# Performance work log

Measured on AMD Instinct MI355X. Metric: run time of the kernel, lower is better.

Reference implementation:

```python
import jax, jax.numpy as jnp
import numpy as np

B = 4             # graphs per batch
POS_RANGE = 240.0 # pos lives in [0, 240)^3
VOXELS = (20.0, 30.0, 50.0, 80.0)
NEG = -1e30


def _basis(u):
    # open B-spline basis, degree 1, kernel_size 2, dim 3 -> 8 weights per edge
    cols = []
    for k in range(8):
        w = (u[:, 0] if k & 4 else 1.0 - u[:, 0])
        w = w * (u[:, 1] if k & 2 else 1.0 - u[:, 1])
        w = w * (u[:, 2] if k & 1 else 1.0 - u[:, 2])
        cols.append(w)
    return jnp.stack(cols, axis=1)  # [E, 8]


def _cartesian(pos, src, dst, emask):
    # T.Cartesian(cat=False, norm=True): rel pos scaled into [0,1]
    rel = pos[src] - pos[dst]
    m = jnp.max(jnp.where(emask[:, None], jnp.abs(rel), 0.0))
    return rel / (2.0 * jnp.maximum(m, 1e-9)) + 0.5


def _spline_conv(x, src, dst, pseudo, emask, W, Wr, b, n_nodes):
    # out_i = mean_{j->i} sum_k B_k(u_ij) x_j W_k + x_i Wr + b
    basis = _basis(pseudo) * emask[:, None].astype(x.dtype)  # [E,8]
    xk = jnp.einsum('ni,kio->nko', x, W)                     # [N,8,O]
    msg = basis[:, 0, None] * xk[src, 0]
    for k in range(1, 8):
        msg = msg + basis[:, k, None] * xk[src, k]           # [E,O]
    agg = jax.ops.segment_sum(msg, dst, num_segments=n_nodes)
    deg = jax.ops.segment_sum(emask.astype(x.dtype), dst, num_segments=n_nodes)
    return agg / jnp.maximum(deg, 1.0)[:, None] + x @ Wr + b


def _voxel_ids(pos, batch, vs):
    G = int(np.ceil(POS_RANGE / vs))
    c = jnp.clip(jnp.floor(pos / vs).astype(jnp.int64), 0, G - 1)
    cell = (c[:, 0] * G + c[:, 1]) * G + c[:, 2]
    return batch * (G ** 3) + cell, G ** 3


def _max_pool(x, pos, batch, valid, src, dst, emask, vs):
    # voxel-grid max pooling: nodes become fixed voxel cells (empty cells masked)
    nid, ncells = _voxel_ids(pos, batch, vs)
    n_new = B * ncells
    xm = jnp.where(valid[:, None], x, NEG)
    x_p = jax.ops.segment_max(xm, nid, num_segments=n_new)
    cnt = jax.ops.segment_sum(valid.astype(x.dtype), nid, num_segments=n_new)
    v_new = cnt > 0
    x_p = jnp.where(v_new[:, None], x_p, 0.0)
    pos_p = jax.ops.segment_sum(pos * valid[:, None].astype(pos.dtype), nid, num_segments=n_new)
    pos_p = pos_p / jnp.maximum(cnt, 1.0)[:, None]
    batch_p = jnp.arange(n_new, dtype=jnp.int64) // ncells
    # coarsen edges: remap to cells, drop self loops, coalesce at fixed size
    s2, d2 = nid[src], nid[dst]
    sent = n_new * n_new
    key = jnp.where(emask & (s2 != d2), s2 * n_new + d2, sent)
    uk = jnp.unique(key, size=key.shape[0], fill_value=sent)
    em = uk != sent
    uk = jnp.where(em, uk, 0)
    return x_p, pos_p, batch_p, v_new, uk // n_new, uk % n_new, em


def setup_inputs():
    key = jax.random.key(0)
    ks = jax.random.split(key, 24)
    NP, DEG = 5000, 8
    N = B * NP
    E = N * DEG
    x = jax.random.normal(ks[0], (N, 1), dtype=jnp.float32)
    pos = jax.random.uniform(ks[1], (N, 3), dtype=jnp.float32) * POS_RANGE
    src = jnp.repeat(jnp.arange(N, dtype=jnp.int64), DEG)
    delta = jax.random.randint(ks[2], (E,), 1, 100, dtype=jnp.int64)
    dst = (src // NP) * NP + (src % NP + delta) % NP   # intra-graph edges
    edge_index = jnp.stack([src, dst])
    batch = jnp.arange(N, dtype=jnp.int64) // NP
    sizes = [1, 64, 128, 256, 512]
    params = {}
    for l in range(4):
        ci, co = sizes[l], sizes[l + 1]
        params[f'W{l+1}'] = jax.random.normal(ks[3 + 3 * l], (8, ci, co), dtype=jnp.float32) / np.sqrt(8.0 * ci)
        params[f'Wr{l+1}'] = jax.random.normal(ks[4 + 3 * l], (ci, co), dtype=jnp.float32) / np.sqrt(float(ci))
        params[f'b{l+1}'] = jnp.zeros((co,), dtype=jnp.float32)
    params['fc1_w'] = jax.random.normal(ks[16], (64 * 512, 1024), dtype=jnp.float32) / np.sqrt(64.0 * 512.0)
    params['fc1_b'] = jnp.zeros((1024,), dtype=jnp.float32)
    params['fc2_w'] = jax.random.normal(ks[17], (1024, 1), dtype=jnp.float32) / np.sqrt(1024.0)
    params['fc2_b'] = jnp.zeros((1,), dtype=jnp.float32)
    return dict(x=x, pos=pos, edge_index=edge_index, batch=batch, **params)


def reference(x, pos, edge_index, batch, W1, Wr1, b1, W2, Wr2, b2, W3, Wr3, b3,
              W4, Wr4, b4, fc1_w, fc1_b, fc2_w, fc2_b):
    src, dst = edge_index[0], edge_index[1]
    n_nodes = x.shape[0]
    valid = jnp.ones((n_nodes,), dtype=bool)
    emask = jnp.ones((src.shape[0],), dtype=bool)
    Ws = [(W1, Wr1, b1), (W2, Wr2, b2), (W3, Wr3, b3), (W4, Wr4, b4)]
    for l in range(4):
        pseudo = _cartesian(pos, src, dst, emask)
        W, Wr, b = Ws[l]
        x = jax.nn.elu(_spline_conv(x, src, dst, pseudo, emask, W, Wr, b, n_nodes))
        if l < 3:
            x, pos, batch, valid, src, dst, emask = _max_pool(x, pos, batch, valid, src, dst, emask, VOXELS[l])
            n_nodes = x.shape[0]
    # MaxPoolingX(voxel=80, size=64): ceil(240/80)^3 = 27 <= 64 slots per graph
    nid, ncells = _voxel_ids(pos, batch, VOXELS[3])
    cluster = batch * 64 + (nid % ncells)
    xm = jnp.where(valid[:, None], x, NEG)
    xg = jax.ops.segment_max(xm, cluster, num_segments=B * 64)
    xg = jnp.where(xg <= NEG / 2, 0.0, xg)      # empty slots -> 0 (scatter-max default)
    xg = xg.reshape(B, 64 * 512)
    h = jax.nn.elu(xg @ fc1_w + fc1_b)           # dropout = identity (eval mode)
    return jax.nn.elu(h @ fc2_w + fc2_b)         # [B, 1]
```

## Files before the change

kernel.cpp:

```cpp
#include <hip/hip_runtime.h>

static constexpr int E0 = 160000;
static constexpr int NL0 = 20000;
static constexpr int NL1 = 6912;
static constexpr int NL2 = 2048;
static constexpr int NL3 = 500;

typedef short bf16x8 __attribute__((ext_vector_type(8)));
typedef float f32x4 __attribute__((ext_vector_type(4)));

__device__ __forceinline__ unsigned f2ord(float f) {
  unsigned u = __float_as_uint(f);
  return (u & 0x80000000u) ? ~u : (u | 0x80000000u);
}
__device__ __forceinline__ float ord2f(unsigned u) {
  unsigned v = (u & 0x80000000u) ? (u & 0x7fffffffu) : ~u;
  return __uint_as_float(v);
}
__device__ __forceinline__ float eluf(float x) { return x > 0.f ? x : expm1f(x); }
__device__ __forceinline__ void basis8(float u0, float u1, float u2, float* w) {
  float a0 = 1.f - u0, a1 = 1.f - u1, a2 = 1.f - u2;
  w[0] = a0*a1*a2; w[1] = a0*a1*u2; w[2] = a0*u1*a2; w[3] = a0*u1*u2;
  w[4] = u0*a1*a2; w[5] = u0*a1*u2; w[6] = u0*u1*a2; w[7] = u0*u1*u2;
}
__device__ __forceinline__ unsigned short f2b(float f) {
  unsigned u = __float_as_uint(f);
  return (unsigned short)((u + 0x7fffu + ((u >> 16) & 1u)) >> 16);
}
__device__ __forceinline__ float b2f(unsigned short h) {
  return __uint_as_float(((unsigned)h) << 16);
}
__device__ __forceinline__ int clampi(int v, int lo, int hi) {
  return v < lo ? lo : (v > hi ? hi : v);
}

__device__ __forceinline__ void mfma_tile(const unsigned short* __restrict__ Ah,
    const unsigned short* __restrict__ Al, const unsigned short* __restrict__ Bh,
    const unsigned short* __restrict__ Bl, int M, long K, int m0, int n0,
    int kbeg, int ksl, char* smem, f32x4* acc) {
  auto Ash = (unsigned short (*)[40])(smem);
  auto Asl = (unsigned short (*)[40])(smem + 5120);
  auto Bsh = (unsigned short (*)[40])(smem + 10240);
  auto Bsl = (unsigned short (*)[40])(smem + 15360);
  int t = threadIdx.x;
  int r = t >> 2, sg = (t & 3) * 8;
  int w = t >> 6, lane = t & 63;
  int ar = (w << 4) + (lane & 15), kq = (lane >> 4) << 3;
  for (int kt = 0; kt < ksl; kt += 32) {
    bf16x8 va = {}, vl = {};
    if (m0 + r < M) {
      long ga = (long)(m0 + r) * K + kbeg + kt + sg;
      va = *(const bf16x8*)&Ah[ga];
      vl = *(const bf16x8*)&Al[ga];
    }
    *(bf16x8*)&Ash[r][sg] = va;
    *(bf16x8*)&Asl[r][sg] = vl;
    long gb = (long)(n0 + r) * K + kbeg + kt + sg;
    *(bf16x8*)&Bsh[r][sg] = *(const bf16x8*)&Bh[gb];
    *(bf16x8*)&Bsl[r][sg] = *(const bf16x8*)&Bl[gb];
    __syncthreads();
    bf16x8 ah = *(const bf16x8*)&Ash[ar][kq];
    bf16x8 al = *(const bf16x8*)&Asl[ar][kq];
    #pragma unroll
    for (int nt = 0; nt < 4; nt++) {
      int br = (nt << 4) + (lane & 15);
      bf16x8 bh = *(const bf16x8*)&Bsh[br][kq];
      bf16x8 bl = *(const bf16x8*)&Bsl[br][kq];
      acc[nt] = __builtin_amdgcn_mfma_f32_16x16x32_bf16(al, bh, acc[nt], 0, 0, 0);
      acc[nt] = __builtin_amdgcn_mfma_f32_16x16x32_bf16(ah, bl, acc[nt], 0, 0, 0);
      acc[nt] = __builtin_amdgcn_mfma_f32_16x16x32_bf16(ah, bh, acc[nt], 0, 0, 0);
    }
    __syncthreads();
  }
}

__global__ __launch_bounds__(256)
void k_prep(const int* __restrict__ src0, const int* __restrict__ dst0,
            const float* __restrict__ pos0, const float* __restrict__ x0,
            int* __restrict__ degi, int4* __restrict__ erec0u, float* __restrict__ mbuf,
            const float* __restrict__ W1, const float* __restrict__ Wr1, float* __restrict__ wc1,
            const float* __restrict__ W2, const float* __restrict__ Wr2,
            const float* __restrict__ W3, const float* __restrict__ Wr3,
            const float* __restrict__ W4, const float* __restrict__ Wr4,
            unsigned short* __restrict__ w2h, unsigned short* __restrict__ w2l,
            unsigned short* __restrict__ w3h, unsigned short* __restrict__ w3l,
            unsigned short* __restrict__ w4h, unsigned short* __restrict__ w4l) {
  __shared__ __align__(16) float T[64][65];
  __shared__ float red[4];
  int tid = blockIdx.x * 256 + threadIdx.x, gsz = gridDim.x * 256;
  float v = 0.f;
  for (int e = tid; e < E0; e += gsz) {
    int s = src0[e], d = dst0[e];
    atomicAdd(&degi[d], 1);
    float r0 = pos0[s*3]   - pos0[d*3];
    float r1 = pos0[s*3+1] - pos0[d*3+1];
    float r2 = pos0[s*3+2] - pos0[d*3+2];
    erec0u[e] = make_int4(__float_as_int(x0[s]), __float_as_int(r0),
                          __float_as_int(r1), __float_as_int(r2));
    v = fmaxf(v, fmaxf(fabsf(r0), fmaxf(fabsf(r1), fabsf(r2))));
  }
  #pragma unroll
  for (int off = 32; off; off >>= 1) v = fmaxf(v, __shfl_down(v, off, 64));
  if ((threadIdx.x & 63) == 0) red[threadIdx.x >> 6] = v;
  __syncthreads();
  if (threadIdx.x == 0)
    atomicMax((unsigned*)mbuf,
              __float_as_uint(fmaxf(fmaxf(red[0], red[1]), fmaxf(red[2], red[3]))));
  for (int b = blockIdx.x; b < 378; b += gridDim.x) {
    const float *W, *Wr; unsigned short *oh, *ol; int K, N, kt, nt;
    if (b < 18)      { W = W2; Wr = Wr2; oh = w2h; ol = w2l; K = 576;  N = 128; kt = b / 2; nt = b % 2; }
    else if (b < 90) { int q = b - 18; W = W3; Wr = Wr3; oh = w3h; ol = w3l; K = 1152; N = 256; kt = q / 4; nt = q % 4; }
    else             { int q = b - 90; W = W4; Wr = Wr4; oh = w4h; ol = w4l; K = 2304; N = 512; kt = q / 8; nt = q % 8; }
    int k0 = kt * 64, n0 = nt * 64, KW = K - K / 9;
    __syncthreads();
    for (int i = threadIdx.x; i < 4096; i += 256) {
      int kk = i >> 6, nn = i & 63, k = k0 + kk;
      T[kk][nn] = (k < KW) ? W[(long)k * N + n0 + nn] : Wr[(long)(k - KW) * N + n0 + nn];
    }
    __syncthreads();
    for (int i = threadIdx.x; i < 4096; i += 256) {
      int nn = i >> 6, kk = i & 63;
      float vv = T[kk][nn];
      unsigned short hu = f2b(vv), lu = f2b(vv - b2f(hu));
      long o = (long)(n0 + nn) * K + k0 + kk;
      oh[o] = hu; ol[o] = lu;
    }
  }
  if (blockIdx.x == 0)
    for (int i = threadIdx.x; i < 576; i += 256)
      wc1[i] = (i < 512) ? W1[i] : Wr1[i - 512];
}

__global__ void k_alloc(int* __restrict__ degi, int* __restrict__ rowbeg,
                        int* __restrict__ rowlen, int* __restrict__ cursor,
                        int* __restrict__ ctr, int N) {
  int n = blockIdx.x * 256 + threadIdx.x;
  if (n >= N) return;
  int len = degi[n];
  int st = atomicAdd(ctr, len);
  rowbeg[n] = st; cursor[n] = st; rowlen[n] = len; degi[n] = 0;
}

__global__ void k_scat(const int4* __restrict__ eu, const int* __restrict__ du,
                       const int* __restrict__ ecnt, int ecap,
                       int* __restrict__ cursor, int4* __restrict__ es) {
  int n = ecnt ? *ecnt : ecap;
  for (int e = blockIdx.x * 256 + threadIdx.x; e < n; e += gridDim.x * 256) {
    int p = atomicAdd(&cursor[du[e]], 1);
    es[p] = eu[e];
  }
}

__global__ __launch_bounds__(256)
void k_l1a(const int4* __restrict__ erec, const int* __restrict__ rowbeg,
           const int* __restrict__ rowlen, const float* __restrict__ mbuf,
           float* __restrict__ ysg) {
  int t = threadIdx.x;
  int d = blockIdx.x * 32 + (t >> 3);
  if (d >= NL0) return;
  int sub = t & 7;
  float inv = 0.5f / fmaxf(mbuf[0], 1e-9f);
  int beg = rowbeg[d], len = rowlen[d], end = beg + len;
  float acc[8] = {};
  for (int j = beg + sub; j < end; j += 8) {
    int4 rc = erec[j];
    float xv = __int_as_float(rc.x);
    float w[8];
    basis8(__int_as_float(rc.y) * inv + 0.5f, __int_as_float(rc.z) * inv + 0.5f,
           __int_as_float(rc.w) * inv + 0.5f, w);
    #pragma unroll
    for (int k = 0; k < 8; k++) acc[k] += w[k] * xv;
  }
  #pragma unroll
  for (int m = 1; m < 8; m <<= 1)
    #pragma unroll
    for (int k = 0; k < 8; k++) acc[k] += __shfl_xor(acc[k], m, 64);
  if (sub == 0) {
    float sc = 1.f / fmaxf((float)len, 1.f);
    float4 o0 = make_float4(acc[0]*sc, acc[1]*sc, acc[2]*sc, acc[3]*sc);
    float4 o1 = make_float4(acc[4]*sc, acc[5]*sc, acc[6]*sc, acc[7]*sc);
    *(float4*)&ysg[d*8]     = o0;
    *(float4*)&ysg[d*8 + 4] = o1;
  }
}

__global__ __launch_bounds__(256)
void k_l1b(const float* __restrict__ ysg, const float* __restrict__ x0,
           const float* __restrict__ pos0, const float* __restrict__ wc1,
           const float* __restrict__ b1,
           unsigned* __restrict__ pord1, float* __restrict__ cnt1,
           float* __restrict__ possum1, int* __restrict__ nid) {
  int wv = threadIdx.x >> 6, lane = threadIdx.x & 63;
  int d = blockIdx.x * 4 + wv;
  if (d >= NL0) return;
  float wcol[9];
  #pragma unroll
  for (int k = 0; k < 8; k++) wcol[k] = wc1[k * 64 + lane];
  wcol[8] = wc1[512 + lane];
  float4 a0 = *(const float4*)&ysg[d*8];
  float4 a1 = *(const float4*)&ysg[d*8 + 4];
  float v = b1[lane] + x0[d] * wcol[8]
          + a0.x * wcol[0] + a0.y * wcol[1] + a0.z * wcol[2] + a0.w * wcol[3]
          + a1.x * wcol[4] + a1.y * wcol[5] + a1.z * wcol[6] + a1.w * wcol[7];
  v = eluf(v);
  float pd0 = pos0[d*3], pd1 = pos0[d*3+1], pd2 = pos0[d*3+2];
  int c0 = clampi((int)floorf(pd0 / 20.f), 0, 11);
  int c1 = clampi((int)floorf(pd1 / 20.f), 0, 11);
  int c2 = clampi((int)floorf(pd2 / 20.f), 0, 11);
  int id = (d / 5000) * 1728 + (c0 * 12 + c1) * 12 + c2;
  atomicMax(&pord1[(long)id * 64 + lane], f2ord(v));
  if (lane == 0) {
    nid[d] = id;
    atomicAdd(&cnt1[id], 1.f);
    atomicAdd(&possum1[id*3],   pd0);
    atomicAdd(&possum1[id*3+1], pd1);
    atomicAdd(&possum1[id*3+2], pd2);
  }
}

__global__ __launch_bounds__(256)
void k_pedge(const int4* __restrict__ erecf, const int* __restrict__ srcf,
             const int* __restrict__ dstf, const int* __restrict__ ecntf, int ecap,
             const int* __restrict__ nid, int Nn, unsigned* __restrict__ bitmap,
             int4* __restrict__ erecu, int* __restrict__ dstu, int* __restrict__ ecntc,
             int* __restrict__ degi, const float* __restrict__ possum,
             const float* __restrict__ cnt, float* __restrict__ mo) {
  __shared__ float red[4];
  int n = ecntf ? *ecntf : ecap;
  int lane = threadIdx.x & 63;
  int stride = gridDim.x * 256;
  float vmax = 0.f;
  for (int base = blockIdx.x * 256; base < n; base += stride) {
    int e = base + threadIdx.x;
    bool win = false;
    int s2 = 0, d2 = 0;
    float r0 = 0.f, r1 = 0.f, r2 = 0.f;
    if (e < n) {
      int sL = erecf ? erecf[e].x : srcf[e];
      int dL = dstf[e];
      s2 = nid[sL]; d2 = nid[dL];
      if (s2 != d2) {
        float ics = 1.f / fmaxf(cnt[s2], 1.f), icd = 1.f / fmaxf(cnt[d2], 1.f);
        r0 = possum[s2*3]   * ics - possum[d2*3]   * icd;
        r1 = possum[s2*3+1] * ics - possum[d2*3+1] * icd;
        r2 = possum[s2*3+2] * ics - possum[d2*3+2] * icd;
        vmax = fmaxf(vmax, fmaxf(fabsf(r0), fmaxf(fabsf(r1), fabsf(r2))));
        unsigned key = (unsigned)s2 * (unsigned)Nn + (unsigned)d2;
        unsigned bit = 1u << (key & 31);
        unsigned old = atomicOr(&bitmap[key >> 5], bit);
        win = !(old & bit);
      }
    }
    unsigned long long mask = __ballot(win);
    if (mask) {
      int leader = __ffsll((unsigned long long)mask) - 1;
      int bq = 0;
      if (lane == leader) bq = atomicAdd(ecntc, __popcll(mask));
      bq = __shfl(bq, leader, 64);
      if (win) {
        int q = bq + __popcll(mask & ((1ULL << lane) - 1ULL));
        erecu[q] = make_int4(s2, __float_as_int(r0), __float_as_int(r1), __float_as_int(r2));
        dstu[q] = d2;
        atomicAdd(&degi[d2], 1);
      }
    }
  }
  #pragma unroll
  for (int off = 32; off; off >>= 1) vmax = fmaxf(vmax, __shfl_down(vmax, off, 64));
  if ((threadIdx.x & 63) == 0) red[threadIdx.x >> 6] = vmax;
  __syncthreads();
  if (threadIdx.x == 0)
    atomicMax((unsigned*)mo,
              __float_as_uint(fmaxf(fmaxf(red[0], red[1]), fmaxf(red[2], red[3]))));
}

template<int ES>
__global__ __launch_bounds__(256)
void k_gather(const unsigned* __restrict__ pordc, const int4* __restrict__ erec,
              const int* __restrict__ rowbeg, const int* __restrict__ rowlen,
              const float* __restrict__ mbuf,
              unsigned short* __restrict__ ysh, unsigned short* __restrict__ ysl,
              int N, int Ci, int nchunk) {
  __shared__ float comb[4][64][8];
  int wv = threadIdx.x >> 6, lane = threadIdx.x & 63;
  int gw = blockIdx.x * 4 + wv;
  int job = gw / ES, sub = gw % ES;
  int d = job / nchunk, ch = job % nchunk;
  bool active = d < N;
  float inv = 0.5f / fmaxf(mbuf[0], 1e-9f);
  int co = ch * 64 + lane;
  float acc[8] = {};
  int beg = 0, len = 0;
  if (active) {
    beg = rowbeg[d]; len = rowlen[d];
    int end = beg + len;
    int j = beg + sub;
    for (; j + 3 * ES < end; j += 4 * ES) {
      int4 ra = erec[j], rb = erec[j + ES], rc = erec[j + 2 * ES], rd = erec[j + 3 * ES];
      float xa = ord2f(pordc[(long)ra.x * Ci + co]);
      float xb = ord2f(pordc[(long)rb.x * Ci + co]);
      float xc = ord2f(pordc[(long)rc.x * Ci + co]);
      float xd = ord2f(pordc[(long)rd.x * Ci + co]);
      float wa[8], wb[8], wc[8], wd[8];
      basis8(__int_as_float(ra.y) * inv + 0.5f, __int_as_float(ra.z) * inv + 0.5f,
             __int_as_float(ra.w) * inv + 0.5f, wa);
      basis8(__int_as_float(rb.y) * inv + 0.5f, __int_as_float(rb.z) * inv + 0.5f,
             __int_as_float(rb.w) * inv + 0.5f, wb);
      basis8(__int_as_float(rc.y) * inv + 0.5f, __int_as_float(rc.z) * inv + 0.5f,
             __int_as_float(rc.w) * inv + 0.5f, wc);
      basis8(__int_as_float(rd.y) * inv + 0.5f, __int_as_float(rd.z) * inv + 0.5f,
             __int_as_float(rd.w) * inv + 0.5f, wd);
      #pragma unroll
      for (int k = 0; k < 8; k++)
        acc[k] += wa[k] * xa + wb[k] * xb + wc[k] * xc + wd[k] * xd;
    }
    for (; j < end; j += ES) {
      int4 ra = erec[j];
      float xa = ord2f(pordc[(long)ra.x * Ci + co]);
      float wa[8];
      basis8(__int_as_float(ra.y) * inv + 0.5f, __int_as_float(ra.z) * inv + 0.5f,
             __int_as_float(ra.w) * inv + 0.5f, wa);
      #pragma unroll
      for (int k = 0; k < 8; k++) acc[k] += wa[k] * xa;
    }
  }
  if (ES > 1) {
    #pragma unroll
    for (int k = 0; k < 8; k++) comb[wv][lane][k] = acc[k];
    __syncthreads();
    if (sub != 0 || !active) return;
    #pragma unroll
    for (int s = 1; s < ES; s++)
      #pragma unroll
      for (int k = 0; k < 8; k++) acc[k] += comb[wv + s][lane][k];
  } else if (!active) return;
  float sc = 1.f / fmaxf((float)len, 1.f);
  long row = (long)d * 9 * Ci;
  #pragma unroll
  for (int k = 0; k < 8; k++) {
    float v = acc[k] * sc;
    unsigned short hu = f2b(v);
    ysh[row + k * Ci + co] = hu;
    ysl[row + k * Ci + co] = f2b(v - b2f(hu));
  }
  unsigned od = pordc[(long)d * Ci + co];
  float xdv = (od == 0u) ? 0.f : ord2f(od);
  unsigned short hu = f2b(xdv);
  ysh[row + 8 * Ci + co] = hu;
  ysl[row + 8 * Ci + co] = f2b(xdv - b2f(hu));
}

__global__ __launch_bounds__(256)
void k_gemmpool(const unsigned short* __restrict__ ysh, const unsigned short* __restrict__ ysl,
                const unsigned short* __restrict__ Bh, const unsigned short* __restrict__ Bl,
                int M, int N, int K, const float* __restrict__ bias,
                const float* __restrict__ possum, const float* __restrict__ cnt,
                int div, float vs, int G, int NC,
                unsigned* __restrict__ pordn, float* __restrict__ cntn,
                float* __restrict__ possumn, int* __restrict__ nid) {
  __shared__ __align__(16) char smem[20480];
  int nbx = N >> 6;
  int bx = blockIdx.x % nbx, by = blockIdx.x / nbx;
  int m0 = by * 64, n0 = bx * 64;
  f32x4 acc[4] = {};
  mfma_tile(ysh, ysl, Bh, Bl, M, K, m0, n0, 0, K, smem, acc);
  int w = threadIdx.x >> 6, lane = threadIdx.x & 63;
  int row0 = m0 + (w << 4) + ((lane >> 4) << 2);
  int colb = n0 + (lane & 15);
  #pragma unroll
  for (int q = 0; q < 4; q++) {
    int gm = row0 + q;
    float c = cnt[gm];
    float ic = 1.f / fmaxf(c, 1.f);
    float p0 = possum[gm*3] * ic, p1 = possum[gm*3+1] * ic, p2 = possum[gm*3+2] * ic;
    int c0 = clampi((int)floorf(p0 / vs), 0, G - 1);
    int c1 = clampi((int)floorf(p1 / vs), 0, G - 1);
    int c2 = clampi((int)floorf(p2 / vs), 0, G - 1);
    int id = (gm / div) * NC + (c0 * G + c1) * G + c2;
    bool vl = c > 0.f;
    if (bx == 0 && (lane & 15) == 0) {
      nid[gm] = id;
      if (vl) {
        atomicAdd(&cntn[id], 1.f);
        atomicAdd(&possumn[id*3],   p0);
        atomicAdd(&possumn[id*3+1], p1);
        atomicAdd(&possumn[id*3+2], p2);
      }
    }
    if (vl) {
      #pragma unroll
      for (int nt = 0; nt < 4; nt++) {
        int col = colb + nt * 16;
        float v = eluf(acc[nt][q] + bias[col]);
        atomicMax(&pordn[(long)id * N + col], f2ord(v));
      }
    }
  }
}

__global__ __launch_bounds__(256)
void k_gemm4(const unsigned short* __restrict__ ysh, const unsigned short* __restrict__ ysl,
             const unsigned short* __restrict__ Bh, const unsigned short* __restrict__ Bl,
             float* __restrict__ Cp) {
  __shared__ __align__(16) char smem[20480];
  int z = blockIdx.x >> 6, rem = blockIdx.x & 63, bx = rem & 7, by = rem >> 3;
  int m0 = by * 64, n0 = bx * 64;
  f32x4 acc[4] = {};
  mfma_tile(ysh, ysl, Bh, Bl, 500, 2304, m0, n0, z * 576, 576, smem, acc);
  float* Co = Cp + (long)z * 256000;
  int w = threadIdx.x >> 6, lane = threadIdx.x & 63;
  int row0 = m0 + (w << 4) + ((lane >> 4) << 2);
  int colb = n0 + (lane & 15);
  #pragma unroll
  for (int nt = 0; nt < 4; nt++)
    #pragma unroll
    for (int q = 0; q < 4; q++) {
      int gm = row0 + q;
      if (gm < 500) Co[(long)gm * 512 + colb + nt * 16] = acc[nt][q];
    }
}

__global__ void k_reduce4(const float* __restrict__ Cp, const float* __restrict__ b4,
                          const float* __restrict__ possum3, const float* __restrict__ cnt3,
                          unsigned* __restrict__ xg) {
  int idx = blockIdx.x * 256 + threadIdx.x;
  if (idx >= 256000) return;
  int n = idx >> 9, o = idx & 511;
  float s = Cp[idx] + Cp[idx + 256000] + Cp[idx + 512000] + Cp[idx + 768000];
  float v = eluf(s + b4[o]);
  float c = cnt3[n];
  if (c <= 0.f) return;
  float ic = 1.f / c;
  float p0 = possum3[n*3] * ic, p1 = possum3[n*3+1] * ic, p2 = possum3[n*3+2] * ic;
  int c0 = clampi((int)floorf(p0 / 80.f), 0, 2);
  int c1 = clampi((int)floorf(p1 / 80.f), 0, 2);
  int c2 = clampi((int)floorf(p2 / 80.f), 0, 2);
  int cl = (n / 125) * 64 + (c0 * 3 + c1) * 3 + c2;
  atomicMax(&xg[(long)cl * 512 + o], f2ord(v));
}

__global__ __launch_bounds__(128)
void k_fc1(const unsigned* __restrict__ xg_ord, const float* __restrict__ w,
           float* __restrict__ h) {
  int cellhalf = blockIdx.x >> 3, jb = blockIdx.x & 7;
  int cell = cellhalf >> 1, half = cellhalf & 1;
  int j = jb * 128 + threadIdx.x;
  __shared__ float xs[4][256];
  for (int q = threadIdx.x; q < 1024; q += 128) {
    int b = q >> 8, ci = q & 255;
    unsigned o = xg_ord[((b * 64 + cell) << 9) + half * 256 + ci];
    xs[b][ci] = (o == 0u) ? 0.f : ord2f(o);
  }
  __syncthreads();
  float a0 = 0, a1 = 0, a2 = 0, a3 = 0;
  int cbase = cell * 512 + half * 256;
  for (int ci = 0; ci < 256; ci++) {
    float ww = w[(long)(cbase + ci) * 1024 + j];
    a0 += xs[0][ci] * ww; a1 += xs[1][ci] * ww;
    a2 += xs[2][ci] * ww; a3 += xs[3][ci] * ww;
  }
  atomicAdd(&h[j], a0);        atomicAdd(&h[1024 + j], a1);
  atomicAdd(&h[2048 + j], a2); atomicAdd(&h[3072 + j], a3);
}

__global__ void k_fc2(const float* __restrict__ h, const float* __restrict__ fb1,
                      const float* __restrict__ w, const float* __restrict__ b,
                      float* __restrict__ out) {
  int bb = blockIdx.x, t = threadIdx.x;
  float a = 0;
  for (int j = t; j < 1024; j += 256) a += eluf(h[bb * 1024 + j] + fb1[j]) * w[j];
  for (int off = 32; off; off >>= 1) a += __shfl_down(a, off, 64);
  __shared__ float red[4];
  int lane = t & 63, wv = t >> 6;
  if (lane == 0) red[wv] = a;
  __syncthreads();
  if (t == 0) out[bb] = eluf(red[0] + red[1] + red[2] + red[3] + b[0]);
}

extern "C" void kernel_launch(void* const* d_in, const int* in_sizes, int n_in,
                              void* d_out, int out_size, void* d_ws, size_t ws_size,
                              hipStream_t stream) {
  const float* x0   = (const float*)d_in[0];
  const float* pos0 = (const float*)d_in[1];
  const int*   ei   = (const int*)d_in[2];
  const float* W1 = (const float*)d_in[4],  *Wr1 = (const float*)d_in[5],  *b1 = (const float*)d_in[6];
  const float* W2 = (const float*)d_in[7],  *Wr2 = (const float*)d_in[8],  *b2 = (const float*)d_in[9];
  const float* W3 = (const float*)d_in[10], *Wr3 = (const float*)d_in[11], *b3 = (const float*)d_in[12];
  const float* W4 = (const float*)d_in[13], *Wr4 = (const float*)d_in[14], *b4 = (const float*)d_in[15];
  const float* fw1 = (const float*)d_in[16], *fb1 = (const float*)d_in[17];
  const float* fw2 = (const float*)d_in[18], *fb2 = (const float*)d_in[19];
  float* out = (float*)d_out;
  const int* src0 = ei;
  const int* dst0 = ei + E0;

  char* ws = (char*)d_ws;
  size_t off = 0;
  auto alloc = [&](size_t bytes) -> void* {
    off = (off + 255) & ~(size_t)255;
    void* q = ws + off; off += bytes; return q;
  };
  int4* erec0u = (int4*)alloc((size_t)E0 * 16);
  int4* erec_s = (int4*)alloc((size_t)E0 * 16);
  int4* eu_a   = (int4*)alloc((size_t)E0 * 16);
  int4* eu_b   = (int4*)alloc((size_t)E0 * 16);
  int* du_a = (int*)alloc(E0 * 4);
  int* du_b = (int*)alloc(E0 * 4);
  int* nid  = (int*)alloc(NL0 * 4);
  int* rowbeg = (int*)alloc(NL0 * 4);
  int* rowlen = (int*)alloc(NL0 * 4);
  int* cursor = (int*)alloc(NL0 * 4);
  float* ysg = (float*)alloc((size_t)NL0 * 8 * 4);
  unsigned short* ysh = (unsigned short*)alloc((size_t)NL1 * 576 * 2);
  unsigned short* ysl = (unsigned short*)alloc((size_t)NL1 * 576 * 2);
  float* wc1 = (float*)alloc(576 * 4);
  unsigned short* w2h = (unsigned short*)alloc((size_t)576 * 128 * 2);
  unsigned short* w2l = (unsigned short*)alloc((size_t)576 * 128 * 2);
  unsigned short* w3h = (unsigned short*)alloc((size_t)1152 * 256 * 2);
  unsigned short* w3l = (unsigned short*)alloc((size_t)1152 * 256 * 2);
  unsigned short* w4h = (unsigned short*)alloc((size_t)2304 * 512 * 2);
  unsigned short* w4l = (unsigned short*)alloc((size_t)2304 * 512 * 2);
  float* Cp = (float*)alloc((size_t)4 * 256000 * 4);
  char* z0 = (char*)alloc(0);
  unsigned* pord1 = (unsigned*)alloc((size_t)NL1 * 64 * 4);
  unsigned* pord2 = (unsigned*)alloc((size_t)NL2 * 128 * 4);
  unsigned* pord3 = (unsigned*)alloc((size_t)NL3 * 256 * 4);
  unsigned* xg    = (unsigned*)alloc((size_t)4 * 64 * 512 * 4);
  float* cnt1 = (float*)alloc(NL1 * 4);
  float* cnt2 = (float*)alloc(NL2 * 4);
  float* cnt3 = (float*)alloc(NL3 * 4);
  float* possum1 = (float*)alloc(NL1 * 12);
  float* possum2 = (float*)alloc(NL2 * 12);
  float* possum3 = (float*)alloc(NL3 * 12);
  size_t bm1w = ((size_t)NL1 * NL1 + 31) / 32;
  size_t bm2w = ((size_t)NL2 * NL2 + 31) / 32;
  size_t bm3w = ((size_t)NL3 * NL3 + 31) / 32;
  unsigned* bm1 = (unsigned*)alloc(bm1w * 4);
  unsigned* bm2 = (unsigned*)alloc(bm2w * 4);
  unsigned* bm3 = (unsigned*)alloc(bm3w * 4);
  int* degi = (int*)alloc(NL0 * 4);
  float* mbuf = (float*)alloc(64);
  int* ecnt = (int*)(mbuf + 8);
  int* ctr  = (int*)(mbuf + 12);
  float* h = (float*)alloc(4096 * 4);
  char* zend = (char*)alloc(0);
  size_t zbytes = (size_t)(zend - z0);
  (void)ws_size; (void)in_sizes; (void)n_in; (void)out_size;

  auto cdiv = [](long a, long b) { return (int)((a + b - 1) / b); };

  hipMemsetAsync(z0, 0, zbytes, stream);

  k_prep<<<512, 256, 0, stream>>>(src0, dst0, pos0, x0, degi, erec0u, mbuf,
                                  W1, Wr1, wc1, W2, Wr2, W3, Wr3, W4, Wr4,
                                  w2h, w2l, w3h, w3l, w4h, w4l);
  k_alloc<<<cdiv(NL0, 256), 256, 0, stream>>>(degi, rowbeg, rowlen, cursor, ctr + 0, NL0);
  k_scat<<<512, 256, 0, stream>>>(erec0u, dst0, nullptr, E0, cursor, erec_s);
  k_l1a<<<cdiv(NL0, 32), 256, 0, stream>>>(erec_s, rowbeg, rowlen, mbuf, ysg);
  k_l1b<<<cdiv(NL0, 4), 256, 0, stream>>>(ysg, x0, pos0, wc1, b1, pord1, cnt1, possum1, nid);
  k_pedge<<<512, 256, 0, stream>>>(nullptr, src0, dst0, nullptr, E0, nid, NL1, bm1,
                                   eu_a, du_a, ecnt + 0, degi, possum1, cnt1, mbuf + 1);
  k_alloc<<<cdiv(NL1, 256), 256, 0, stream>>>(degi, rowbeg, rowlen, cursor, ctr + 1, NL1);
  k_scat<<<512, 256, 0, stream>>>(eu_a, du_a, ecnt + 0, E0, cursor, erec_s);
  k_gather<1><<<cdiv(NL1, 4), 256, 0, stream>>>(pord1, erec_s, rowbeg, rowlen, mbuf + 1,
                                                ysh, ysl, NL1, 64, 1);
  k_gemmpool<<<(128 / 64) * (NL1 / 64), 256, 0, stream>>>(
      ysh, ysl, w2h, w2l, NL1, 128, 576, b2, possum1, cnt1,
      1728, 30.f, 8, 512, pord2, cnt2, possum2, nid);
  k_pedge<<<512, 256, 0, stream>>>(eu_a, nullptr, du_a, ecnt + 0, E0, nid, NL2, bm2,
                                   eu_b, du_b, ecnt + 1, degi, possum2, cnt2, mbuf + 2);
  k_alloc<<<cdiv(NL2, 256), 256, 0, stream>>>(degi, rowbeg, rowlen, cursor, ctr + 2, NL2);
  k_scat<<<512, 256, 0, stream>>>(eu_b, du_b, ecnt + 1, E0, cursor, erec_s);
  k_gather<2><<<cdiv(NL2 * 2 * 2, 4), 256, 0, stream>>>(pord2, erec_s, rowbeg, rowlen, mbuf + 2,
                                                        ysh, ysl, NL2, 128, 2);
  k_gemmpool<<<(256 / 64) * (NL2 / 64), 256, 0, stream>>>(
      ysh, ysl, w3h, w3l, NL2, 256, 1152, b3, possum2, cnt2,
      512, 50.f, 5, 125, pord3, cnt3, possum3, nid);
  k_pedge<<<512, 256, 0, stream>>>(eu_b, nullptr, du_b, ecnt + 1, E0, nid, NL3, bm3,
                                   eu_a, du_a, ecnt + 2, degi, possum3, cnt3, mbuf + 3);
  k_alloc<<<cdiv(NL3, 256), 256, 0, stream>>>(degi, rowbeg, rowlen, cursor, ctr + 3, NL3);
  k_scat<<<512, 256, 0, stream>>>(eu_a, du_a, ecnt + 2, E0, cursor, erec_s);
  k_gather<4><<<cdiv(NL3 * 4 * 4, 4), 256, 0, stream>>>(pord3, erec_s, rowbeg, rowlen, mbuf + 3,
                                                        ysh, ysl, NL3, 256, 4);
  k_gemm4<<<256, 256, 0, stream>>>(ysh, ysl, w4h, w4l, Cp);
  k_reduce4<<<cdiv(256000, 256), 256, 0, stream>>>(Cp, b4, possum3, cnt3, xg);
  k_fc1<<<27 * 2 * 8, 128, 0, stream>>>(xg, fw1, h);
  k_fc2<<<4, 256, 0, stream>>>(h, fb1, fw2, fb2, out);
}
```

Measured before the change: 412.2 us.

## Fuse layer-1 kernels, split-K reduce into gemm4, and distribute buffer zeroing

Merges the two layer-1 kernels into one, staging per-node aggregates and weights in shared memory. The split-K reduction and final pooling move into the last-arriving block of k_gemm4, which is detected with an atomic counter. The large memset is broken up so each pooling buffer is zeroed inside an earlier kernel (k_prep, k_gather). The gather kernels also get more chunks per node, and fc1 runs twice as many blocks with half the K each. Together these cut launches and the big upfront memset, at the cost of extra work in other kernels and reliance on threadfence ordering.

After: 417.7 us. Within noise of the previous version (+1.3%).

```diff
diff --git a/kernel.cpp b/kernel.cpp
--- a/kernel.cpp
+++ b/kernel.cpp
@@ -78,6 +78,7 @@
 void k_prep(const int* __restrict__ src0, const int* __restrict__ dst0,
             const float* __restrict__ pos0, const float* __restrict__ x0,
             int* __restrict__ degi, int4* __restrict__ erec0u, float* __restrict__ mbuf,
+            unsigned* __restrict__ zA, long zAw,
             const float* __restrict__ W1, const float* __restrict__ Wr1, float* __restrict__ wc1,
             const float* __restrict__ W2, const float* __restrict__ Wr2,
             const float* __restrict__ W3, const float* __restrict__ Wr3,
@@ -87,9 +88,11 @@
             unsigned short* __restrict__ w4h, unsigned short* __restrict__ w4l) {
   __shared__ __align__(16) float T[64][65];
   __shared__ float red[4];
-  int tid = blockIdx.x * 256 + threadIdx.x, gsz = gridDim.x * 256;
+  int tid = blockIdx.x * 256 + threadIdx.x;
+  long gsz = (long)gridDim.x * 256;
+  for (long i = tid; i < zAw; i += gsz) zA[i] = 0u;
   float v = 0.f;
-  for (int e = tid; e < E0; e += gsz) {
+  for (int e = tid; e < E0; e += (int)gsz) {
     int s = src0[e], d = dst0[e];
     atomicAdd(&degi[d], 1);
     float r0 = pos0[s*3]   - pos0[d*3];
@@ -152,69 +155,73 @@
 }
 
 __global__ __launch_bounds__(256)
-void k_l1a(const int4* __restrict__ erec, const int* __restrict__ rowbeg,
-           const int* __restrict__ rowlen, const float* __restrict__ mbuf,
-           float* __restrict__ ysg) {
+void k_l1(const int4* __restrict__ erec, const int* __restrict__ rowbeg,
+          const int* __restrict__ rowlen, const float* __restrict__ mbuf,
+          const float* __restrict__ x0, const float* __restrict__ pos0,
+          const float* __restrict__ wc1, const float* __restrict__ b1,
+          unsigned* __restrict__ pord1, float* __restrict__ cnt1,
+          float* __restrict__ possum1, int* __restrict__ nid) {
+  __shared__ float wls[576];
+  __shared__ float b1s[64];
+  __shared__ float ys[32][12];
   int t = threadIdx.x;
+  for (int i = t; i < 576; i += 256) wls[i] = wc1[i];
+  if (t < 64) b1s[t] = b1[t];
   int d = blockIdx.x * 32 + (t >> 3);
-  if (d >= NL0) return;
   int sub = t & 7;
   float inv = 0.5f / fmaxf(mbuf[0], 1e-9f);
-  int beg = rowbeg[d], len = rowlen[d], end = beg + len;
-  float acc[8] = {};
-  for (int j = beg + sub; j < end; j += 8) {
-    int4 rc = erec[j];
-    float xv = __int_as_float(rc.x);
-    float w[8];
-    basis8(__int_as_float(rc.y) * inv + 0.5f, __int_as_float(rc.z) * inv + 0.5f,
-           __int_as_float(rc.w) * inv + 0.5f, w);
+  if (d < NL0) {
+    int beg = rowbeg[d], len = rowlen[d], end = beg + len;
+    float acc[8] = {};
+    for (int j = beg + sub; j < end; j += 8) {
+      int4 rc = erec[j];
+      float xv = __int_as_float(rc.x);
+      float w[8];
+      basis8(__int_as_float(rc.y) * inv + 0.5f, __int_as_float(rc.z) * inv + 0.5f,
+             __int_as_float(rc.w) * inv + 0.5f, w);
+      #pragma unroll
+      for (int k = 0; k < 8; k++) acc[k] += w[k] * xv;
+    }
     #pragma unroll
-    for (int k = 0; k < 8; k++) acc[k] += w[k] * xv;
-  }
-  #pragma unroll
-  for (int m = 1; m < 8; m <<= 1)
-    #pragma unroll
-    for (int k = 0; k < 8; k++) acc[k] += __shfl_xor(acc[k], m, 64);
-  if (sub == 0) {
-    float sc = 1.f / fmaxf((float)len, 1.f);
-    float4 o0 = make_float4(acc[0]*sc, acc[1]*sc, acc[2]*sc, acc[3]*sc);
-    float4 o1 = make_float4(acc[4]*sc, acc[5]*sc, acc[6]*sc, acc[7]*sc);
-    *(float4*)&ysg[d*8]     = o0;
-    *(float4*)&ysg[d*8 + 4] = o1;
-  }
-}
-
-__global__ __launch_bounds__(256)
-void k_l1b(const float* __restrict__ ysg, const float* __restrict__ x0,
-           const float* __restrict__ pos0, const float* __restrict__ wc1,
-           const float* __restrict__ b1,
-           unsigned* __restrict__ pord1, float* __restrict__ cnt1,
-           float* __restrict__ possum1, int* __restrict__ nid) {
-  int wv = threadIdx.x >> 6, lane = threadIdx.x & 63;
-  int d = blockIdx.x * 4 + wv;
-  if (d >= NL0) return;
-  float wcol[9];
-  #pragma unroll
-  for (int k = 0; k < 8; k++) wcol[k] = wc1[k * 64 + lane];
-  wcol[8] = wc1[512 + lane];
-  float4 a0 = *(const float4*)&ysg[d*8];
-  float4 a1 = *(const float4*)&ysg[d*8 + 4];
-  float v = b1[lane] + x0[d] * wcol[8]
-          + a0.x * wcol[0] + a0.y * wcol[1] + a0.z * wcol[2] + a0.w * wcol[3]
-          + a1.x * wcol[4] + a1.y * wcol[5] + a1.z * wcol[6] + a1.w * wcol[7];
-  v = eluf(v);
-  float pd0 = pos0[d*3], pd1 = pos0[d*3+1], pd2 = pos0[d*3+2];
-  int c0 = clampi((int)floorf(pd0 / 20.f), 0, 11);
-  int c1 = clampi((int)floorf(pd1 / 20.f), 0, 11);
-  int c2 = clampi((int)floorf(pd2 / 20.f), 0, 11);
-  int id = (d / 5000) * 1728 + (c0 * 12 + c1) * 12 + c2;
-  atomicMax(&pord1[(long)id * 64 + lane], f2ord(v));
-  if (lane == 0) {
-    nid[d] = id;
-    atomicAdd(&cnt1[id], 1.f);
-    atomicAdd(&possum1[id*3],   pd0);
-    atomicAdd(&possum1[id*3+1], pd1);
-    atomicAdd(&possum1[id*3+2], pd2);
+    for (int m = 1; m < 8; m <<= 1)
+      #pragma unroll
+      for (int k = 0; k < 8; k++) acc[k] += __shfl_xor(acc[k], m, 64);
+    if (sub == 0) {
+      float sc = 1.f / fmaxf((float)len, 1.f);
+      int nl = t >> 3;
+      #pragma unroll
+      for (int k = 0; k < 8; k++) ys[nl][k] = acc[k] * sc;
+      ys[nl][8]  = x0[d];
+      ys[nl][9]  = pos0[d*3];
+      ys[nl][10] = pos0[d*3+1];
+      ys[nl][11] = pos0[d*3+2];
+    }
+  }
+  __syncthreads();
+  #pragma unroll 2
+  for (int it = 0; it < 8; it++) {
+    int idx = it * 256 + t;
+    int nl = idx >> 6, ch = idx & 63;
+    int dd = blockIdx.x * 32 + nl;
+    if (dd < NL0) {
+      float v = b1s[ch] + ys[nl][8] * wls[512 + ch];
+      #pragma unroll
+      for (int k = 0; k < 8; k++) v += ys[nl][k] * wls[k * 64 + ch];
+      v = eluf(v);
+      float pd0 = ys[nl][9], pd1 = ys[nl][10], pd2 = ys[nl][11];
+      int c0 = clampi((int)floorf(pd0 / 20.f), 0, 11);
+      int c1 = clampi((int)floorf(pd1 / 20.f), 0, 11);
+      int c2 = clampi((int)floorf(pd2 / 20.f), 0, 11);
+      int id = (dd / 5000) * 1728 + (c0 * 12 + c1) * 12 + c2;
+      atomicMax(&pord1[(long)id * 64 + ch], f2ord(v));
+      if (ch == 0) {
+        nid[dd] = id;
+        atomicAdd(&cnt1[id], 1.f);
+        atomicAdd(&possum1[id*3],   pd0);
+        atomicAdd(&possum1[id*3+1], pd1);
+        atomicAdd(&possum1[id*3+2], pd2);
+      }
+    }
   }
 }
 
@@ -280,7 +287,10 @@
               const int* __restrict__ rowbeg, const int* __restrict__ rowlen,
               const float* __restrict__ mbuf,
               unsigned short* __restrict__ ysh, unsigned short* __restrict__ ysl,
-              int N, int Ci, int nchunk) {
+              int N, int Ci, int nchunk,
+              unsigned* __restrict__ zp, long zw) {
+  for (long i = (long)blockIdx.x * 256 + threadIdx.x; i < zw;
+       i += (long)gridDim.x * 256) zp[i] = 0u;
   __shared__ float comb[4][64][8];
   int wv = threadIdx.x >> 6, lane = threadIdx.x & 63;
   int gw = blockIdx.x * 4 + wv;
@@ -401,8 +411,11 @@
 __global__ __launch_bounds__(256)
 void k_gemm4(const unsigned short* __restrict__ ysh, const unsigned short* __restrict__ ysl,
              const unsigned short* __restrict__ Bh, const unsigned short* __restrict__ Bl,
-             float* __restrict__ Cp) {
+             float* __restrict__ Cp, int* __restrict__ done,
+             const float* __restrict__ b4, const float* __restrict__ possum3,
+             const float* __restrict__ cnt3, unsigned* __restrict__ xg) {
   __shared__ __align__(16) char smem[20480];
+  __shared__ int flag;
   int z = blockIdx.x >> 6, rem = blockIdx.x & 63, bx = rem & 7, by = rem >> 3;
   int m0 = by * 64, n0 = bx * 64;
   f32x4 acc[4] = {};
@@ -418,43 +431,53 @@
       int gm = row0 + q;
       if (gm < 500) Co[(long)gm * 512 + colb + nt * 16] = acc[nt][q];
     }
-}
-
-__global__ void k_reduce4(const float* __restrict__ Cp, const float* __restrict__ b4,
-                          const float* __restrict__ possum3, const float* __restrict__ cnt3,
-                          unsigned* __restrict__ xg) {
-  int idx = blockIdx.x * 256 + threadIdx.x;
-  if (idx >= 256000) return;
-  int n = idx >> 9, o = idx & 511;
-  float s = Cp[idx] + Cp[idx + 256000] + Cp[idx + 512000] + Cp[idx + 768000];
-  float v = eluf(s + b4[o]);
-  float c = cnt3[n];
-  if (c <= 0.f) return;
-  float ic = 1.f / c;
-  float p0 = possum3[n*3] * ic, p1 = possum3[n*3+1] * ic, p2 = possum3[n*3+2] * ic;
-  int c0 = clampi((int)floorf(p0 / 80.f), 0, 2);
-  int c1 = clampi((int)floorf(p1 / 80.f), 0, 2);
-  int c2 = clampi((int)floorf(p2 / 80.f), 0, 2);
-  int cl = (n / 125) * 64 + (c0 * 3 + c1) * 3 + c2;
-  atomicMax(&xg[(long)cl * 512 + o], f2ord(v));
+  __threadfence();
+  if (threadIdx.x == 0) flag = atomicAdd(&done[rem], 1);
+  __syncthreads();
+  if (flag != 3) return;
+  __threadfence();
+  #pragma unroll
+  for (int q = 0; q < 4; q++) {
+    int gm = row0 + q;
+    if (gm >= 500) continue;
+    float c = cnt3[gm];
+    if (c <= 0.f) continue;
+    float ic = 1.f / c;
+    float p0 = possum3[gm*3] * ic, p1 = possum3[gm*3+1] * ic, p2 = possum3[gm*3+2] * ic;
+    int c0 = clampi((int)floorf(p0 / 80.f), 0, 2);
+    int c1 = clampi((int)floorf(p1 / 80.f), 0, 2);
+    int c2 = clampi((int)floorf(p2 / 80.f), 0, 2);
+    int cl = (gm / 125) * 64 + (c0 * 3 + c1) * 3 + c2;
+    #pragma unroll
+    for (int nt = 0; nt < 4; nt++) {
+      int col = colb + nt * 16;
+      long idx = (long)gm * 512 + col;
+      float s = Cp[idx] + Cp[idx + 256000] + Cp[idx + 512000] + Cp[idx + 768000];
+      float v = eluf(s + b4[col]);
+      atomicMax(&xg[(long)cl * 512 + col], f2ord(v));
+    }
+  }
 }
 
 __global__ __launch_bounds__(128)
 void k_fc1(const unsigned* __restrict__ xg_ord, const float* __restrict__ w,
            float* __restrict__ h) {
-  int cellhalf = blockIdx.x >> 3, jb = blockIdx.x & 7;
+  int cellhalf = blockIdx.x >> 4;
+  int r = blockIdx.x & 15;
+  int jb = r >> 1, ciq = r & 1;
   int cell = cellhalf >> 1, half = cellhalf & 1;
   int j = jb * 128 + threadIdx.x;
-  __shared__ float xs[4][256];
-  for (int q = threadIdx.x; q < 1024; q += 128) {
-    int b = q >> 8, ci = q & 255;
-    unsigned o = xg_ord[((b * 64 + cell) << 9) + half * 256 + ci];
+  __shared__ float xs[4][128];
+  for (int q = threadIdx.x; q < 512; q += 128) {
+    int b = q >> 7, ci = q & 127;
+    unsigned o = xg_ord[((b * 64 + cell) << 9) + half * 256 + ciq * 128 + ci];
     xs[b][ci] = (o == 0u) ? 0.f : ord2f(o);
   }
   __syncthreads();
   float a0 = 0, a1 = 0, a2 = 0, a3 = 0;
-  int cbase = cell * 512 + half * 256;
-  for (int ci = 0; ci < 256; ci++) {
+  int cbase = cell * 512 + half * 256 + ciq * 128;
+  #pragma unroll 2
+  for (int ci = 0; ci < 128; ci++) {
     float ww = w[(long)(cbase + ci) * 1024 + j];
     a0 += xs[0][ci] * ww; a1 += xs[1][ci] * ww;
     a2 += xs[2][ci] * ww; a3 += xs[3][ci] * ww;
@@ -509,7 +532,6 @@
   int* rowbeg = (int*)alloc(NL0 * 4);
   int* rowlen = (int*)alloc(NL0 * 4);
   int* cursor = (int*)alloc(NL0 * 4);
-  float* ysg = (float*)alloc((size_t)NL0 * 8 * 4);
   unsigned short* ysh = (unsigned short*)alloc((size_t)NL1 * 576 * 2);
   unsigned short* ysl = (unsigned short*)alloc((size_t)NL1 * 576 * 2);
   float* wc1 = (float*)alloc(576 * 4);
@@ -520,49 +542,60 @@
   unsigned short* w4h = (unsigned short*)alloc((size_t)2304 * 512 * 2);
   unsigned short* w4l = (unsigned short*)alloc((size_t)2304 * 512 * 2);
   float* Cp = (float*)alloc((size_t)4 * 256000 * 4);
-  char* z0 = (char*)alloc(0);
+  char* tz = (char*)alloc(0);
+  float* mbuf = (float*)alloc(32);
+  int* ecnt = (int*)alloc(32);
+  int* ctr  = (int*)alloc(32);
+  int* done = (int*)alloc(64 * 4);
+  int* degi = (int*)alloc(NL0 * 4);
+  float* h  = (float*)alloc(4096 * 4);
+  char* tzend = (char*)alloc(0);
+  size_t tzbytes = (size_t)(tzend - tz);
+  char* zA = (char*)alloc(0);
+  size_t bm1w = ((size_t)NL1 * NL1 + 31) / 32;
+  unsigned* bm1 = (unsigned*)alloc(bm1w * 4);
   unsigned* pord1 = (unsigned*)alloc((size_t)NL1 * 64 * 4);
+  float* cnt1 = (float*)alloc(NL1 * 4);
+  float* possum1 = (float*)alloc(NL1 * 12);
+  char* zAend = (char*)alloc(0);
+  long zAw = (long)(zAend - zA) / 4;
+  char* zB = (char*)alloc(0);
+  size_t bm2w = ((size_t)NL2 * NL2 + 31) / 32;
+  unsigned* bm2 = (unsigned*)alloc(bm2w * 4);
   unsigned* pord2 = (unsigned*)alloc((size_t)NL2 * 128 * 4);
+  float* cnt2 = (float*)alloc(NL2 * 4);
+  float* possum2 = (float*)alloc(NL2 * 12);
+  char* zBend = (char*)alloc(0);
+  long zBw = (long)(zBend - zB) / 4;
+  char* zC = (char*)alloc(0);
+  size_t bm3w = ((size_t)NL3 * NL3 + 31) / 32;
+  unsigned* bm3 = (unsigned*)alloc(bm3w * 4);
   unsigned* pord3 = (unsigned*)alloc((size_t)NL3 * 256 * 4);
-  unsigned* xg    = (unsigned*)alloc((size_t)4 * 64 * 512 * 4);
-  float* cnt1 = (float*)alloc(NL1 * 4);
-  float* cnt2 = (float*)alloc(NL2 * 4);
   float* cnt3 = (float*)alloc(NL3 * 4);
-  float* possum1 = (float*)alloc(NL1 * 12);
-  float* possum2 = (float*)alloc(NL2 * 12);
   float* possum3 = (float*)alloc(NL3 * 12);
-  size_t bm1w = ((size_t)NL1 * NL1 + 31) / 32;
-  size_t bm2w = ((size_t)NL2 * NL2 + 31) / 32;
-  size_t bm3w = ((size_t)NL3 * NL3 + 31) / 32;
-  unsigned* bm1 = (unsigned*)alloc(bm1w * 4);
-  unsigned* bm2 = (unsigned*)alloc(bm2w * 4);
-  unsigned* bm3 = (unsigned*)alloc(bm3w * 4);
-  int* degi = (int*)alloc(NL0 * 4);
-  float* mbuf = (float*)alloc(64);
-  int* ecnt = (int*)(mbuf + 8);
-  int* ctr  = (int*)(mbuf + 12);
-  float* h = (float*)alloc(4096 * 4);
-  char* zend = (char*)alloc(0);
-  size_t zbytes = (size_t)(zend - z0);
+  char* zCend = (char*)alloc(0);
+  long zCw = (long)(zCend - zC) / 4;
+  unsigned* xg = (unsigned*)alloc((size_t)4 * 64 * 512 * 4);
+  long zDw = 4 * 64 * 512;
   (void)ws_size; (void)in_sizes; (void)n_in; (void)out_size;
 
   auto cdiv = [](long a, long b) { return (int)((a + b - 1) / b); };
 
-  hipMemsetAsync(z0, 0, zbytes, stream);
-
-  k_prep<<<512, 256, 0, stream>>>(src0, dst0, pos0, x0, degi, erec0u, mbuf,
+  hipMemsetAsync(tz, 0, tzbytes, stream);
+
+  k_prep<<<512, 256, 0, stream>>>(src0, dst0, pos0, x0, degi, erec0u, mbuf, (unsigned*)zA, zAw,
                                   W1, Wr1, wc1, W2, Wr2, W3, Wr3, W4, Wr4,
                                   w2h, w2l, w3h, w3l, w4h, w4l);
   k_alloc<<<cdiv(NL0, 256), 256, 0, stream>>>(degi, rowbeg, rowlen, cursor, ctr + 0, NL0);
   k_scat<<<512, 256, 0, stream>>>(erec0u, dst0, nullptr, E0, cursor, erec_s);
-  k_l1a<<<cdiv(NL0, 32), 256, 0, stream>>>(erec_s, rowbeg, rowlen, mbuf, ysg);
-  k_l1b<<<cdiv(NL0, 4), 256, 0, stream>>>(ysg, x0, pos0, wc1, b1, pord1, cnt1, possum1, nid);
+  k_l1<<<cdiv(NL0, 32), 256, 0, stream>>>(erec_s, rowbeg, rowlen, mbuf, x0, pos0,
+                                          wc1, b1, pord1, cnt1, possum1, nid);
   k_pedge<<<512, 256, 0, stream>>>(nullptr, src0, dst0, nullptr, E0, nid, NL1, bm1,
                                    eu_a, du_a, ecnt + 0, degi, possum1, cnt1, mbuf + 1);
   k_alloc<<<cdiv(NL1, 256), 256, 0, stream>>>(degi, rowbeg, rowlen, cursor, ctr + 1, NL1);
   k_scat<<<512, 256, 0, stream>>>(eu_a, du_a, ecnt + 0, E0, cursor, erec_s);
-  k_gather<1><<<cdiv(NL1, 4), 256, 0, stream>>>(pord1, erec_s, rowbeg, rowlen, mbuf + 1,
-                                                ysh, ysl, NL1, 64, 1);
+  k_gather<2><<<cdiv((long)NL1 * 2, 4), 256, 0, stream>>>(pord1, erec_s, rowbeg, rowlen, mbuf + 1,
+                                                          ysh, ysl, NL1, 64, 1, (unsigned*)zB, zBw);
   k_gemmpool<<<(128 / 64) * (NL1 / 64), 256, 0, stream>>>(
       ysh, ysl, w2h, w2l, NL1, 128, 576, b2, possum1, cnt1,
       1728, 30.f, 8, 512, pord2, cnt2, possum2, nid);
@@ -570,8 +603,8 @@
                                    eu_b, du_b, ecnt + 1, degi, possum2, cnt2, mbuf + 2);
   k_alloc<<<cdiv(NL2, 256), 256, 0, stream>>>(degi, rowbeg, rowlen, cursor, ctr + 2, NL2);
   k_scat<<<512, 256, 0, stream>>>(eu_b, du_b, ecnt + 1, E0, cursor, erec_s);
-  k_gather<2><<<cdiv(NL2 * 2 * 2, 4), 256, 0, stream>>>(pord2, erec_s, rowbeg, rowlen, mbuf + 2,
-                                                        ysh, ysl, NL2, 128, 2);
+  k_gather<4><<<cdiv((long)NL2 * 2 * 4, 4), 256, 0, stream>>>(pord2, erec_s, rowbeg, rowlen, mbuf + 2,
+                                                              ysh, ysl, NL2, 128, 2, (unsigned*)zC, zCw);
   k_gemmpool<<<(256 / 64) * (NL2 / 64), 256, 0, stream>>>(
       ysh, ysl, w3h, w3l, NL2, 256, 1152, b3, possum2, cnt2,
       512, 50.f, 5, 125, pord3, cnt3, possum3, nid);
@@ -579,10 +612,9 @@
                                    eu_a, du_a, ecnt + 2, degi, possum3, cnt3, mbuf + 3);
   k_alloc<<<cdiv(NL3, 256), 256, 0, stream>>>(degi, rowbeg, rowlen, cursor, ctr + 3, NL3);
   k_scat<<<512, 256, 0, stream>>>(eu_a, du_a, ecnt + 2, E0, cursor, erec_s);
-  k_gather<4><<<cdiv(NL3 * 4 * 4, 4), 256, 0, stream>>>(pord3, erec_s, rowbeg, rowlen, mbuf + 3,
-                                                        ysh, ysl, NL3, 256, 4);
-  k_gemm4<<<256, 256, 0, stream>>>(ysh, ysl, w4h, w4l, Cp);
-  k_reduce4<<<cdiv(256000, 256), 256, 0, stream>>>(Cp, b4, possum3, cnt3, xg);
-  k_fc1<<<27 * 2 * 8, 128, 0, stream>>>(xg, fw1, h);
+  k_gather<4><<<cdiv((long)NL3 * 4 * 4, 4), 256, 0, stream>>>(pord3, erec_s, rowbeg, rowlen, mbuf + 3,
+                                                              ysh, ysl, NL3, 256, 4, xg, zDw);
+  k_gemm4<<<256, 256, 0, stream>>>(ysh, ysl, w4h, w4l, Cp, done, b4, possum3, cnt3, xg);
+  k_fc1<<<27 * 2 * 8 * 2, 128, 0, stream>>>(xg, fw1, h);
   k_fc2<<<4, 256, 0, stream>>>(h, fb1, fw2, fb2, out);
 }
```
